# Kernel tuning notes

Measured on AMD Instinct MI355X. Metric: run time of the kernel, lower is better.

The kernel has to match this reference:

```python
import jax, jax.numpy as jnp
import numpy as np

B, L, C, H, W = 2, 4, 128, 48, 176
RATIO, DS = 0.4, 4.0   # voxel_size[0], downsample_rate
NUM_ITER = 2


def _make_pairwise_t(key):
    k1, k2 = jax.random.split(key)
    theta = jax.random.uniform(k1, (B, L, L), minval=-0.2, maxval=0.2)
    t = jax.random.uniform(k2, (B, L, L, 2), minval=-8.0, maxval=8.0)  # meters
    c, s = jnp.cos(theta), jnp.sin(theta)
    T = jnp.zeros((B, L, L, 4, 4), dtype=jnp.float32)
    T = T.at[..., 0, 0].set(c).at[..., 0, 1].set(-s)
    T = T.at[..., 1, 0].set(s).at[..., 1, 1].set(c)
    T = T.at[..., 0, 3].set(t[..., 0]).at[..., 1, 3].set(t[..., 1])
    T = T.at[..., 2, 2].set(1.0).at[..., 3, 3].set(1.0)
    d = jnp.arange(L)
    T = T.at[:, d, d].set(jnp.eye(4, dtype=jnp.float32))  # self-transform = identity
    return T


def setup_inputs():
    key = jax.random.key(0)
    ks = jax.random.split(key, 8)
    x = jax.random.normal(ks[0], (B, L, C, H, W), dtype=jnp.float32)
    record_len = jnp.array([L, L - 1], dtype=jnp.int32)
    mask = (jnp.arange(L)[None, :] < record_len[:, None]).astype(jnp.float32)
    pairwise_t_matrix = _make_pairwise_t(ks[1])
    W_msg = jax.random.normal(ks[2], (C, 2 * C, 3, 3), dtype=jnp.float32) * 0.021
    b_msg = jnp.zeros((C,), dtype=jnp.float32)
    W_gates = jax.random.normal(ks[3], (2 * C, 3 * C, 3, 3), dtype=jnp.float32) * 0.017
    b_gates = jnp.zeros((2 * C,), dtype=jnp.float32)
    W_can = jax.random.normal(ks[4], (C, 3 * C, 3, 3), dtype=jnp.float32) * 0.017
    b_can = jnp.zeros((C,), dtype=jnp.float32)
    W_mlp = jax.random.normal(ks[5], (C, C), dtype=jnp.float32) * 0.088
    b_mlp = jnp.zeros((C,), dtype=jnp.float32)
    return {"x": x, "mask": mask, "pairwise_t_matrix": pairwise_t_matrix,
            "record_len": record_len, "W_msg": W_msg, "b_msg": b_msg,
            "W_gates": W_gates, "b_gates": b_gates, "W_can": W_can,
            "b_can": b_can, "W_mlp": W_mlp, "b_mlp": b_mlp}


def _conv2d(x, w, b):
    y = jax.lax.conv_general_dilated(x, w, (1, 1), 'SAME',
                                     dimension_numbers=('NCHW', 'OIHW', 'NCHW'))
    return y + b[None, :, None, None]


def _affine_inv(T):
    # T: (..., 4, 4) neighbor->ego transform. Returns (..., 2, 3) inverse pixel
    # affine (maps dst pixel -> src pixel), i.e. get_discretized_transformation_matrix
    # + rotation-about-center + translation, then inverted (kornia warp_affine semantics).
    R = T[..., :2, :2]
    t = T[..., :2, 3] / (RATIO * DS)             # translation in pixels
    c = jnp.array([W / 2.0, H / 2.0], dtype=T.dtype)
    full_t = c - jnp.einsum('...ij,j->...i', R, c) + t   # (..., 2)
    det = R[..., 0, 0] * R[..., 1, 1] - R[..., 0, 1] * R[..., 1, 0]
    Rinv = jnp.stack([jnp.stack([R[..., 1, 1], -R[..., 0, 1]], -1),
                      jnp.stack([-R[..., 1, 0], R[..., 0, 0]], -1)], -2) / det[..., None, None]
    tinv = -jnp.einsum('...ij,...j->...i', Rinv, full_t)
    return jnp.concatenate([Rinv, tinv[..., None]], axis=-1)


def _warp_one(img, A):
    # img: (C, H, W); A: (2, 3) dst->src pixel map. Bilinear, zeros padding.
    ys, xs = jnp.meshgrid(jnp.arange(H, dtype=img.dtype),
                          jnp.arange(W, dtype=img.dtype), indexing='ij')
    sx = A[0, 0] * xs + A[0, 1] * ys + A[0, 2]
    sy = A[1, 0] * xs + A[1, 1] * ys + A[1, 2]
    x0 = jnp.floor(sx); y0 = jnp.floor(sy)
    wx1 = sx - x0; wy1 = sy - y0
    def gather(xi, yi):
        valid = ((xi >= 0) & (xi <= W - 1) & (yi >= 0) & (yi <= H - 1)).astype(img.dtype)
        xc = jnp.clip(xi, 0, W - 1).astype(jnp.int32)
        yc = jnp.clip(yi, 0, H - 1).astype(jnp.int32)
        return img[:, yc, xc] * valid
    return (gather(x0, y0) * (1 - wx1) * (1 - wy1)
            + gather(x0 + 1, y0) * wx1 * (1 - wy1)
            + gather(x0, y0 + 1) * (1 - wx1) * wy1
            + gather(x0 + 1, y0 + 1) * wx1 * wy1)


def _forward(x, mask, pairwise_t_matrix, record_len,
             W_msg, b_msg, W_gates, b_gates, W_can, b_can, W_mlp, b_mlp):
    # Ainv[b, j, i] warps neighbor j into ego i's frame; reorder to (b, i, j).
    Ainv = _affine_inv(pairwise_t_matrix)                      # (B, L, L, 2, 3)
    Ainv_bij = jnp.transpose(Ainv, (0, 2, 1, 3, 4)).reshape(-1, 2, 3)
    warp_v = jax.vmap(_warp_one)
    ones_img = jnp.ones((1, H, W), dtype=x.dtype)
    roi = jax.vmap(lambda A: _warp_one(ones_img, A))(Ainv_bij)  # (B*L*L, 1, H, W)
    com_mask = roi.reshape(B, L, L, 1, H, W) * mask[:, None, :, None, None, None]
    rec = record_len.astype(x.dtype)[:, None, None, None, None]
    feat = x
    for _ in range(NUM_ITER):
        nb = jnp.broadcast_to(feat[:, None], (B, L, L, C, H, W)).reshape(-1, C, H, W)
        warped = warp_v(nb, Ainv_bij).reshape(B, L, L, C, H, W)
        ego = jnp.broadcast_to(feat[:, :, None], (B, L, L, C, H, W))
        msg_in = jnp.concatenate([warped, ego], axis=3).reshape(-1, 2 * C, H, W)
        msg = _conv2d(msg_in, W_msg, b_msg).reshape(B, L, L, C, H, W) * com_mask
        agg = jnp.sum(msg, axis=2) / rec                        # mean over N valid cavs
        # ConvGRU, single layer / single step, zero-initialized hidden state
        gru_in = jnp.concatenate([feat, agg], axis=2).reshape(-1, 2 * C, H, W)
        h = jnp.zeros((B * L, C, H, W), dtype=x.dtype)
        gates = jax.nn.sigmoid(_conv2d(jnp.concatenate([gru_in, h], 1), W_gates, b_gates))
        r, u = jnp.split(gates, 2, axis=1)
        cand = jnp.tanh(_conv2d(jnp.concatenate([gru_in, r * h], 1), W_can, b_can))
        h = (1 - u) * h + u * cand
        feat = h.reshape(B, L, C, H, W)
    out = feat[:, 0]                                            # ego agent of each sample
    return jnp.einsum('bchw,oc->bohw', out, W_mlp) + b_mlp[None, :, None, None]


def reference(x, mask, pairwise_t_matrix, record_len,
              W_msg, b_msg, W_gates, b_gates, W_can, b_can, W_mlp, b_mlp):
    return _forward(x, mask, pairwise_t_matrix, record_len,
                    W_msg, b_msg, W_gates, b_gates, W_can, b_can, W_mlp, b_mlp)
```

## Files before the change

### kernel.cpp

```cpp
#include <hip/hip_runtime.h>
#include <math.h>

#define BB 2
#define LL 4
#define CC 128
#define HH 48
#define WWID 176
#define HW 8448

typedef _Float16 f16;
typedef __attribute__((ext_vector_type(8))) _Float16 f16x8;
typedef __attribute__((ext_vector_type(4))) _Float16 f16x4;
typedef __attribute__((ext_vector_type(2))) _Float16 f16x2;
typedef __attribute__((ext_vector_type(4))) float f32x4;
typedef __attribute__((ext_vector_type(4))) unsigned int u32x4;

__device__ __forceinline__ void ainv_from(const float* __restrict__ t, float* a)
{
    float R00=t[0], R01=t[1], t0=t[3];
    float R10=t[4], R11=t[5], t1=t[7];
    float tx = t0 * 0.625f;
    float ty = t1 * 0.625f;
    const float cx = WWID/2.0f, cy = HH/2.0f;
    float ftx = cx - (R00*cx + R01*cy) + tx;
    float fty = cy - (R10*cx + R11*cy) + ty;
    float det = R00*R11 - R01*R10;
    float inv = 1.0f/det;
    float i00 =  R11*inv, i01 = -R01*inv, i10 = -R10*inv, i11 = R00*inv;
    a[0]=i00; a[1]=i01; a[2]=-(i00*ftx + i01*fty);
    a[3]=i10; a[4]=i11; a[5]=-(i10*ftx + i11*fty);
}

__global__ __launch_bounds__(256)
void prep_kernel(const float* __restrict__ Wm, const float* __restrict__ Wg,
                 const float* __restrict__ Wc, const float* __restrict__ x,
                 const float* __restrict__ T, const float* __restrict__ mask,
                 f16* __restrict__ WmF, f16* __restrict__ WuF, f16* __restrict__ WcF,
                 f16* __restrict__ xT, float* __restrict__ fac)
{
    int bid = blockIdx.x;
    int tid = threadIdx.x;
    if (bid < 3456) {
        int which = bid / 1152;
        const float* src = (which==0) ? Wm : (which==1) ? Wg : Wc;
        f16* dst         = (which==0) ? WmF : (which==1) ? WuF : WcF;
        int oc_off = (which==1) ? 128 : 0;
        int stride = (which==0) ? 256 : 384;
        int idx = (bid % 1152)*256 + tid;
        int j     = idx & 7;
        int hi    = (idx >> 3) & 3;
        int l15   = (idx >> 5) & 15;
        int ocblk = (idx >> 9) & 7;
        int kq    = (idx >> 12) & 7;
        int tap   = idx >> 15;
        int oc  = ocblk*16 + l15;
        int cin = kq*32 + hi*8 + j;
        dst[idx] = (f16)src[((size_t)(oc_off+oc)*stride + cin)*9 + tap];
    } else if (bid < 3720) {
        int g = bid - 3456;
        int bl = g / 33;
        int pix = (g % 33)*256 + tid;
        const float* src = x + (size_t)bl*CC*HW + pix;
        f16* dst = xT + (size_t)bl*HW*CC + (size_t)pix*CC;
        for (int gg = 0; gg < 8; ++gg) {
            f16x8 v0, v1;
            #pragma unroll
            for (int c2 = 0; c2 < 8; ++c2) {
                v0[c2] = (f16)src[(size_t)(gg*16 + c2    )*HW];
                v1[c2] = (f16)src[(size_t)(gg*16 + 8 + c2)*HW];
            }
            *(f16x8*)(dst + gg*16    ) = v0;
            *(f16x8*)(dst + gg*16 + 8) = v1;
        }
    } else {
        int g = bid - 3720;
        int slot = g / 33;
        int pix = (g % 33)*256 + tid;
        int b = slot >> 4, l2 = (slot >> 2) & 3;
        float mk = mask[b*LL + l2];
        float a[6];
        ainv_from(T + slot*16, a);
        float gx = (float)(pix % WWID), gy = (float)(pix / WWID);
        float sx = a[0]*gx + a[1]*gy + a[2];
        float sy = a[3]*gx + a[4]*gy + a[5];
        float x0 = floorf(sx), y0 = floorf(sy);
        float wx = sx-x0, wy = sy-y0;
        int xi=(int)x0, yi=(int)y0;
        bool vx0 = xi>=0 && xi<WWID, vx1 = xi+1>=0 && xi+1<WWID;
        bool vy0 = yi>=0 && yi<HH,   vy1 = yi+1>=0 && yi+1<HH;
        float r = (vx0&&vy0?(1.f-wx)*(1.f-wy):0.f) + (vx1&&vy0?wx*(1.f-wy):0.f)
                + (vx0&&vy1?(1.f-wx)*wy:0.f)       + (vx1&&vy1?wx*wy:0.f);
        fac[(size_t)slot*HW + pix] = r*mk;
    }
}

template<int NM>
__global__ __launch_bounds__(256,3)
void msg_conv_kernel(const f16* __restrict__ featT, const float* __restrict__ T,
                     const float* __restrict__ fac, const float* __restrict__ mask,
                     const int* __restrict__ reclen,
                     const f16* __restrict__ WmF, const float* __restrict__ bm,
                     f16* __restrict__ Pm, int n_l1)
{
    int z = blockIdx.z;
    int b = z / (n_l1*5);
    int rem = z - b*(n_l1*5);
    int l1 = rem / 5, src = rem % 5;
    if (l1 != 0 && mask[b*LL + l1] == 0.f) return;
    bool ego = (src == 4);
    int l2 = ego ? l1 : src;
    if (!ego && mask[b*LL + l2] == 0.f) return;
    bool gather = (!ego) && (l2 != l1);
    int och = blockIdx.y;

    int ty = blockIdx.x / 11, tx = blockIdx.x % 11;
    int y0 = ty*8, x0 = tx*16;
    int tid = threadIdx.x;
    int wid = tid >> 6, lane = tid & 63;
    int wr = wid >> 1, wc = wid & 1;
    int l15 = lane & 15, hi = lane >> 4;

    __shared__ short lt[180*128];
    __shared__ float tw[4][192];
    __shared__ int   tof[4][192];

    const f16* in = featT + (size_t)(b*LL + l2)*HW*CC;

    if (gather) {
        float a6[6];
        ainv_from(T + ((b*LL + l2)*LL + l1)*16, a6);
        float a0=a6[0],a1=a6[1],a2=a6[2],a3=a6[3],a4=a6[4],a5=a6[5];
        for (int r = tid; r < 180; r += 256) {
            int yy = r / 18, xx = r - yy*18;
            int gy = y0 - 1 + yy, gx = x0 - 1 + xx;
            float w00=0.f,w10=0.f,w01=0.f,w11=0.f;
            int o00=0,o10=0,o01=0,o11=0;
            if (gy>=0 && gy<HH && gx>=0 && gx<WWID) {
                float sx = a0*(float)gx + a1*(float)gy + a2;
                float sy = a3*(float)gx + a4*(float)gy + a5;
                float xf = floorf(sx), yf = floorf(sy);
                float wx = sx-xf, wyv = sy-yf;
                int xi=(int)xf, yi=(int)yf;
                bool vx0=xi>=0&&xi<WWID, vx1=xi+1>=0&&xi+1<WWID;
                bool vy0=yi>=0&&yi<HH,   vy1=yi+1>=0&&yi+1<HH;
                int xc0=min(max(xi,0),WWID-1), xc1=min(max(xi+1,0),WWID-1);
                int yc0=min(max(yi,0),HH-1),   yc1=min(max(yi+1,0),HH-1);
                o00=(yc0*WWID+xc0)*CC; o10=(yc0*WWID+xc1)*CC;
                o01=(yc1*WWID+xc0)*CC; o11=(yc1*WWID+xc1)*CC;
                w00=(vx0&&vy0)?(1.f-wx)*(1.f-wyv):0.f;
                w10=(vx1&&vy0)?wx*(1.f-wyv):0.f;
                w01=(vx0&&vy1)?(1.f-wx)*wyv:0.f;
                w11=(vx1&&vy1)?wx*wyv:0.f;
            }
            tw[0][r]=w00; tw[1][r]=w10; tw[2][r]=w01; tw[3][r]=w11;
            tof[0][r]=o00; tof[1][r]=o10; tof[2][r]=o01; tof[3][r]=o11;
        }
        __syncthreads();
        for (int i = tid; i < 180*16; i += 256) {
            int row = i >> 4, cg = i & 15;
            f16 h00=(f16)tw[0][row], h10=(f16)tw[1][row];
            f16 h01=(f16)tw[2][row], h11=(f16)tw[3][row];
            f16x2 W00={h00,h00}, W10={h10,h10}, W01={h01,h01}, W11={h11,h11};
            int o00=tof[0][row], o10=tof[1][row], o01=tof[2][row], o11=tof[3][row];
            f16x8 t00 = *(const f16x8*)(in + o00 + cg*8);
            f16x8 t10 = *(const f16x8*)(in + o10 + cg*8);
            f16x8 t01 = *(const f16x8*)(in + o01 + cg*8);
            f16x8 t11 = *(const f16x8*)(in + o11 + cg*8);
            const f16x2* p00 = (const f16x2*)&t00;
            const f16x2* p10 = (const f16x2*)&t10;
            const f16x2* p01 = (const f16x2*)&t01;
            const f16x2* p11 = (const f16x2*)&t11;
            f16x8 outv;
            f16x2* po = (f16x2*)&outv;
            #pragma unroll
            for (int q=0;q<4;++q)
                po[q] = p00[q]*W00 + p10[q]*W10 + p01[q]*W01 + p11[q]*W11;
            int byte = row*256 + ((cg*16) ^ ((row&7)<<4));
            *(f16x8*)((char*)lt + byte) = outv;
        }
    } else {
        for (int i = tid; i < 180*16; i += 256) {
            int row = i >> 4, cg = i & 15;
            int yy = row / 18, xx = row - yy*18;
            int gy = y0 - 1 + yy, gx = x0 - 1 + xx;
            u32x4 val = {0,0,0,0};
            if (gy>=0 && gy<HH && gx>=0 && gx<WWID)
                val = *(const u32x4*)(in + (size_t)(gy*WWID+gx)*CC + cg*8);
            int byte = row*256 + ((cg*16) ^ ((row&7)<<4));
            *(u32x4*)((char*)lt + byte) = val;
        }
    }
    __syncthreads();

    f32x4 acc[NM][4];
    #pragma unroll
    for (int m=0;m<NM;++m)
        #pragma unroll
        for (int n=0;n<4;++n) acc[m][n] = (f32x4){0.f,0.f,0.f,0.f};

    const int kqbase = ego ? 4 : 0;
    const f16* wlane = WmF + l15*32 + hi*8;
    __builtin_amdgcn_s_setprio(1);
    for (int tap=0; tap<9; ++tap) {
        int dy = tap/3, dx = tap - dy*3;
        #pragma unroll
        for (int kk=0; kk<4; ++kk) {
            const f16* wt = wlane + (size_t)(((tap*8 + kqbase + kk)*8 + och*4 + wr*NM))*512;
            f16x8 av[NM];
            #pragma unroll
            for (int m=0;m<NM;++m)
                av[m] = *(const f16x8*)(wt + m*512);
            f16x8 bv[4];
            #pragma unroll
            for (int n=0;n<4;++n) {
                int pos = (wc*4 + n + dy)*18 + dx + l15;
                int byte = pos*256 + ((kk*64 + hi*16) ^ ((pos&7)<<4));
                bv[n] = *(const f16x8*)((const char*)lt + byte);
            }
            #pragma unroll
            for (int m=0;m<NM;++m)
                #pragma unroll
                for (int n=0;n<4;++n)
                    acc[m][n] = __builtin_amdgcn_mfma_f32_16x16x32_f16(
                        av[m], bv[n], acc[m][n], 0, 0, 0);
        }
    }
    __builtin_amdgcn_s_setprio(0);

    float invrec = 1.0f / (float)reclen[b];
    float fsc[4];
    if (ego) {
        #pragma unroll
        for (int n=0;n<4;++n) fsc[n] = 0.f;
        for (int j=0;j<LL;++j) {
            if (mask[b*LL + j] == 0.f) continue;
            const float* fp = fac + (size_t)(b*16 + j*4 + l1)*HW;
            #pragma unroll
            for (int n=0;n<4;++n)
                fsc[n] += fp[(y0 + wc*4 + n)*WWID + x0 + l15];
        }
    } else {
        const float* fp = fac + (size_t)(b*16 + l2*4 + l1)*HW;
        #pragma unroll
        for (int n=0;n<4;++n)
            fsc[n] = fp[(y0 + wc*4 + n)*WWID + x0 + l15];
    }
    #pragma unroll
    for (int n=0;n<4;++n) fsc[n] *= invrec;

    f16* outp = Pm + (size_t)z*HW*CC;
    #pragma unroll
    for (int m=0;m<NM;++m) {
        int oc = (och*4 + wr*NM + m)*16 + hi*4;
        f32x4 b4 = {0.f,0.f,0.f,0.f};
        if (ego) b4 = *(const f32x4*)(bm + oc);
        #pragma unroll
        for (int n=0;n<4;++n) {
            int pix = (y0 + wc*4 + n)*WWID + x0 + l15;
            f32x4 v = (acc[m][n] + b4) * fsc[n];
            f16x4 h = {(f16)v[0], (f16)v[1], (f16)v[2], (f16)v[3]};
            *(f16x4*)(outp + (size_t)pix*CC + oc) = h;
        }
    }
}

__global__ __launch_bounds__(256)
void reduce_agg_kernel(const f16* __restrict__ Pm, const float* __restrict__ mask,
                       f16* __restrict__ aggT, int n_l1)
{
    int zi = blockIdx.y;
    int b = zi / n_l1, l1 = zi % n_l1;
    if (l1 != 0 && mask[b*LL + l1] == 0.f) return;
    int idx = blockIdx.x*256 + threadIdx.x;
    int pix = idx >> 2, cgq = idx & 3;
    bool act[4];
    #pragma unroll
    for (int j=0;j<LL;++j) act[j] = (mask[b*LL + j] != 0.f);
    size_t off = (size_t)pix*CC + cgq*32;
    const f16* base = Pm + (size_t)(zi*5)*HW*CC + off;
    f16* dst = aggT + (size_t)zi*HW*CC + off;
    for (int cg=0; cg<4; ++cg) {
        float s[8];
        f16x8 e = *(const f16x8*)(base + (size_t)4*HW*CC + cg*8);
        #pragma unroll
        for (int j8=0;j8<8;++j8) s[j8] = (float)e[j8];
        #pragma unroll
        for (int j=0;j<4;++j) {
            if (!act[j]) continue;
            f16x8 p = *(const f16x8*)(base + (size_t)j*HW*CC + cg*8);
            #pragma unroll
            for (int j8=0;j8<8;++j8) s[j8] += (float)p[j8];
        }
        f16x8 o;
        #pragma unroll
        for (int j8=0;j8<8;++j8) o[j8] = (f16)s[j8];
        *(f16x8*)(dst + cg*8) = o;
    }
}

template<int NM>
__global__ __launch_bounds__(256,3)
void gru_conv_kernel(const f16* __restrict__ featT, const f16* __restrict__ aggT,
                     const float* __restrict__ mask,
                     const f16* __restrict__ WuF, const f16* __restrict__ WcF,
                     f16* __restrict__ Pg, int n_l1, int noc)
{
    int z = blockIdx.z;
    int b = z / n_l1, l1 = z % n_l1;
    if (l1 != 0 && mask[b*LL + l1] == 0.f) return;
    int gate = blockIdx.y / noc;
    int och  = blockIdx.y % noc;

    int ty = blockIdx.x / 11, tx = blockIdx.x % 11;
    int y0 = ty*8, x0 = tx*16;
    int tid = threadIdx.x;
    int wid = tid >> 6, lane = tid & 63;
    int wr = wid >> 1, wc = wid & 1;
    int l15 = lane & 15, hi = lane >> 4;

    __shared__ short lt[180*128];

    f32x4 acc[NM][4];
    #pragma unroll
    for (int m=0;m<NM;++m)
        #pragma unroll
        for (int n=0;n<4;++n) acc[m][n] = (f32x4){0.f,0.f,0.f,0.f};

    const f16* WF = (gate==0) ? WuF : WcF;
    const f16* wlane = WF + l15*32 + hi*8;

    for (int s = 0; s < 2; ++s) {
        const f16* in = (s==0) ? featT + (size_t)(b*LL + l1)*HW*CC
                               : aggT  + (size_t)(b*n_l1 + l1)*HW*CC;
        if (s) __syncthreads();
        for (int i = tid; i < 180*16; i += 256) {
            int row = i >> 4, cg = i & 15;
            int yy = row / 18, xx = row - yy*18;
            int gy = y0 - 1 + yy, gx = x0 - 1 + xx;
            u32x4 val = {0,0,0,0};
            if (gy>=0 && gy<HH && gx>=0 && gx<WWID)
                val = *(const u32x4*)(in + (size_t)(gy*WWID+gx)*CC + cg*8);
            int byte = row*256 + ((cg*16) ^ ((row&7)<<4));
            *(u32x4*)((char*)lt + byte) = val;
        }
        __syncthreads();

        int kqbase = s*4;
        __builtin_amdgcn_s_setprio(1);
        for (int tap=0; tap<9; ++tap) {
            int dy = tap/3, dx = tap - dy*3;
            #pragma unroll
            for (int kk=0; kk<4; ++kk) {
                const f16* wt = wlane + (size_t)(((tap*8 + kqbase + kk)*8 + och*4 + wr*NM))*512;
                f16x8 av[NM];
                #pragma unroll
                for (int m=0;m<NM;++m)
                    av[m] = *(const f16x8*)(wt + m*512);
                f16x8 bv[4];
                #pragma unroll
                for (int n=0;n<4;++n) {
                    int pos = (wc*4 + n + dy)*18 + dx + l15;
                    int byte = pos*256 + ((kk*64 + hi*16) ^ ((pos&7)<<4));
                    bv[n] = *(const f16x8*)((const char*)lt + byte);
                }
                #pragma unroll
                for (int m=0;m<NM;++m)
                    #pragma unroll
                    for (int n=0;n<4;++n)
                        acc[m][n] = __builtin_amdgcn_mfma_f32_16x16x32_f16(
                            av[m], bv[n], acc[m][n], 0, 0, 0);
            }
        }
        __builtin_amdgcn_s_setprio(0);
    }

    f16* outp = Pg + ((size_t)(gate*(BB*LL) + z))*HW*CC;
    #pragma unroll
    for (int m=0;m<NM;++m) {
        int oc = (och*4 + wr*NM + m)*16 + hi*4;
        #pragma unroll
        for (int n=0;n<4;++n) {
            int pix = (y0 + wc*4 + n)*WWID + x0 + l15;
            f32x4 v = acc[m][n];
            f16x4 h = {(f16)v[0], (f16)v[1], (f16)v[2], (f16)v[3]};
            *(f16x4*)(outp + (size_t)pix*CC + oc) = h;
        }
    }
}

__global__ __launch_bounds__(256)
void combine_kernel(const f16* __restrict__ Pg, const float* __restrict__ mask,
                    const float* __restrict__ bgU, const float* __restrict__ bc,
                    f16* __restrict__ outT, int n_l1)
{
    int z = blockIdx.y;
    int b = z / n_l1, l1 = z % n_l1;
    if (l1 != 0 && mask[b*LL + l1] == 0.f) return;
    int idx = blockIdx.x*256 + threadIdx.x;
    int pix = idx >> 2, cgq = idx & 3;
    size_t poff = (size_t)pix*CC + cgq*32;
    const f16* U = Pg + ((size_t)(0*(BB*LL) + z))*HW*CC + poff;
    const f16* C = Pg + ((size_t)(1*(BB*LL) + z))*HW*CC + poff;
    f16* dst = outT + (size_t)z*HW*CC + poff;
    for (int cg=0; cg<4; ++cg) {
        f16x8 u8 = *(const f16x8*)(U + cg*8);
        f16x8 c8 = *(const f16x8*)(C + cg*8);
        f16x8 o;
        #pragma unroll
        for (int j=0; j<8; ++j) {
            float uu = (float)u8[j] + bgU[cgq*32 + cg*8 + j];
            float cc = (float)c8[j] + bc[cgq*32 + cg*8 + j];
            float sig = 1.f/(1.f + expf(-uu));
            o[j] = (f16)(sig * tanhf(cc));
        }
        *(f16x8*)(dst + cg*8) = o;
    }
}

__global__ __launch_bounds__(256)
void mlp_kernel(const f16* __restrict__ Pg, const float* __restrict__ bgU,
                const float* __restrict__ bc, const float* __restrict__ Wm,
                const float* __restrict__ bmlp, float* __restrict__ out)
{
    int b = blockIdx.z, oc0 = blockIdx.y*32;
    int pix = blockIdx.x*256 + threadIdx.x;
    size_t poff = (size_t)pix*CC;
    const f16* U = Pg + ((size_t)(0*(BB*LL) + b))*HW*CC + poff;
    const f16* C = Pg + ((size_t)(1*(BB*LL) + b))*HW*CC + poff;
    float acc[32];
    #pragma unroll
    for (int oc=0;oc<32;++oc) acc[oc]=0.f;
    for (int c8 = 0; c8 < 16; ++c8) {
        f16x8 u8 = *(const f16x8*)(U + c8*8);
        f16x8 g8 = *(const f16x8*)(C + c8*8);
        float f[8];
        #pragma unroll
        for (int j=0;j<8;++j) {
            float uu = (float)u8[j] + bgU[c8*8 + j];
            float cc = (float)g8[j] + bc[c8*8 + j];
            float sig = 1.f/(1.f + expf(-uu));
            f[j] = sig * tanhf(cc);
        }
        #pragma unroll
        for (int oc=0; oc<32; ++oc) {
            const float* w = Wm + (size_t)(oc0+oc)*CC + c8*8;
            #pragma unroll
            for (int j=0;j<8;++j) acc[oc] = fmaf(f[j], w[j], acc[oc]);
        }
    }
    #pragma unroll
    for (int oc=0;oc<32;++oc)
        out[((size_t)b*CC + oc0+oc)*HW + pix] = acc[oc] + bmlp[oc0+oc];
}

extern "C" void kernel_launch(void* const* d_in, const int* in_sizes, int n_in,
                              void* d_out, int out_size, void* d_ws, size_t ws_size,
                              hipStream_t stream)
{
    const float* x     = (const float*)d_in[0];
    const float* mask  = (const float*)d_in[1];
    const float* T     = (const float*)d_in[2];
    const int*   recl  = (const int*)  d_in[3];
    const float* Wmsg  = (const float*)d_in[4];
    const float* bmsg  = (const float*)d_in[5];
    const float* Wg    = (const float*)d_in[6];
    const float* bg    = (const float*)d_in[7];
    const float* Wc    = (const float*)d_in[8];
    const float* bc    = (const float*)d_in[9];
    const float* Wmlp  = (const float*)d_in[10];
    const float* bmlp  = (const float*)d_in[11];
    float* out = (float*)d_out;

    char* w = (char*)d_ws;
    f16*   xT   = (f16*)w;            w += (size_t)BB*LL*HW*CC*2;
    float* fac  = (float*)w;          w += (size_t)32*HW*4;
    f16*   WmF  = (f16*)w;            w += (size_t)9*128*256*2;
    f16*   WuF  = (f16*)w;            w += (size_t)9*128*256*2;
    f16*   WcF  = (f16*)w;            w += (size_t)9*128*256*2;
    f16*   Pm   = (f16*)w;            w += (size_t)40*HW*CC*2;
    f16*   Pg   = (f16*)w;            w += (size_t)2*BB*LL*HW*CC*2;
    f16*   aggT = (f16*)w;            w += (size_t)BB*LL*HW*CC*2;
    f16*   f1T  = (f16*)w;            w += (size_t)BB*LL*HW*CC*2;

    prep_kernel<<<4776, 256, 0, stream>>>(Wmsg, Wg, Wc, x, T, mask,
                                          WmF, WuF, WcF, xT, fac);

    msg_conv_kernel<4><<<dim3(66, 1, BB*LL*5), 256, 0, stream>>>(
        xT, T, fac, mask, recl, WmF, bmsg, Pm, LL);
    reduce_agg_kernel<<<dim3(132, BB*LL), 256, 0, stream>>>(Pm, mask, aggT, LL);
    gru_conv_kernel<4><<<dim3(66, 2, BB*LL), 256, 0, stream>>>(
        xT, aggT, mask, WuF, WcF, Pg, LL, 1);
    combine_kernel<<<dim3(132, BB*LL), 256, 0, stream>>>(
        Pg, mask, bg + CC, bc, f1T, LL);

    msg_conv_kernel<2><<<dim3(66, 2, BB*5), 256, 0, stream>>>(
        f1T, T, fac, mask, recl, WmF, bmsg, Pm, 1);
    reduce_agg_kernel<<<dim3(132, BB), 256, 0, stream>>>(Pm, mask, aggT, 1);
    gru_conv_kernel<2><<<dim3(66, 4, BB), 256, 0, stream>>>(
        f1T, aggT, mask, WuF, WcF, Pg, 1, 2);

    mlp_kernel<<<dim3(33, 4, BB), 256, 0, stream>>>(
        Pg, bg + CC, bc, Wmlp, bmlp, out);
}
```

Before: 461.0 us.

## Fuse GRU update and candidate convs with the gate epilogue in one kernel

The GRU conv kernel now computes the update-gate and candidate convolutions together for the same output channels, sharing one LDS input tile. It then applies sigmoid·tanh in the epilogue and writes the new hidden state directly. This removes the separate combine kernel and the round trip of the two pre-activation tensors through global memory, and the final MLP now reads the finished feature map. The NM tiling is halved to keep two accumulator sets within register limits, which changes per-block work and may raise register pressure or lower occupancy.

```diff
diff --git a/kernel.cpp b/kernel.cpp
--- a/kernel.cpp
+++ b/kernel.cpp
@@ -205,7 +205,7 @@
         int dy = tap/3, dx = tap - dy*3;
         #pragma unroll
         for (int kk=0; kk<4; ++kk) {
-            const f16* wt = wlane + (size_t)(((tap*8 + kqbase + kk)*8 + och*4 + wr*NM))*512;
+            const f16* wt = wlane + (size_t)(((tap*8 + kqbase + kk)*8 + och*(2*NM) + wr*NM))*512;
             f16x8 av[NM];
             #pragma unroll
             for (int m=0;m<NM;++m)
@@ -251,7 +251,7 @@
     f16* outp = Pm + (size_t)z*HW*CC;
     #pragma unroll
     for (int m=0;m<NM;++m) {
-        int oc = (och*4 + wr*NM + m)*16 + hi*4;
+        int oc = (och*(2*NM) + wr*NM + m)*16 + hi*4;
         f32x4 b4 = {0.f,0.f,0.f,0.f};
         if (ego) b4 = *(const f32x4*)(bm + oc);
         #pragma unroll
@@ -303,13 +303,13 @@
 void gru_conv_kernel(const f16* __restrict__ featT, const f16* __restrict__ aggT,
                      const float* __restrict__ mask,
                      const f16* __restrict__ WuF, const f16* __restrict__ WcF,
-                     f16* __restrict__ Pg, int n_l1, int noc)
+                     const float* __restrict__ bgU, const float* __restrict__ bc,
+                     f16* __restrict__ outT, int n_l1)
 {
     int z = blockIdx.z;
     int b = z / n_l1, l1 = z % n_l1;
     if (l1 != 0 && mask[b*LL + l1] == 0.f) return;
-    int gate = blockIdx.y / noc;
-    int och  = blockIdx.y % noc;
+    int och = blockIdx.y;
 
     int ty = blockIdx.x / 11, tx = blockIdx.x % 11;
     int y0 = ty*8, x0 = tx*16;
@@ -320,14 +320,17 @@
 
     __shared__ short lt[180*128];
 
-    f32x4 acc[NM][4];
+    f32x4 aU[NM][4], aC[NM][4];
     #pragma unroll
     for (int m=0;m<NM;++m)
         #pragma unroll
-        for (int n=0;n<4;++n) acc[m][n] = (f32x4){0.f,0.f,0.f,0.f};
-
-    const f16* WF = (gate==0) ? WuF : WcF;
-    const f16* wlane = WF + l15*32 + hi*8;
+        for (int n=0;n<4;++n) {
+            aU[m][n] = (f32x4){0.f,0.f,0.f,0.f};
+            aC[m][n] = (f32x4){0.f,0.f,0.f,0.f};
+        }
+
+    const f16* wlaneU = WuF + l15*32 + hi*8;
+    const f16* wlaneC = WcF + l15*32 + hi*8;
 
     for (int s = 0; s < 2; ++s) {
         const f16* in = (s==0) ? featT + (size_t)(b*LL + l1)*HW*CC
@@ -351,11 +354,13 @@
             int dy = tap/3, dx = tap - dy*3;
             #pragma unroll
             for (int kk=0; kk<4; ++kk) {
-                const f16* wt = wlane + (size_t)(((tap*8 + kqbase + kk)*8 + och*4 + wr*NM))*512;
-                f16x8 av[NM];
+                size_t blkoff = (size_t)(((tap*8 + kqbase + kk)*8 + och*(2*NM) + wr*NM))*512;
+                f16x8 avU[NM], avC[NM];
                 #pragma unroll
-                for (int m=0;m<NM;++m)
-                    av[m] = *(const f16x8*)(wt + m*512);
+                for (int m=0;m<NM;++m) {
+                    avU[m] = *(const f16x8*)(wlaneU + blkoff + m*512);
+                    avC[m] = *(const f16x8*)(wlaneC + blkoff + m*512);
+                }
                 f16x8 bv[4];
                 #pragma unroll
                 for (int n=0;n<4;++n) {
@@ -366,81 +371,54 @@
                 #pragma unroll
                 for (int m=0;m<NM;++m)
                     #pragma unroll
-                    for (int n=0;n<4;++n)
-                        acc[m][n] = __builtin_amdgcn_mfma_f32_16x16x32_f16(
-                            av[m], bv[n], acc[m][n], 0, 0, 0);
+                    for (int n=0;n<4;++n) {
+                        aU[m][n] = __builtin_amdgcn_mfma_f32_16x16x32_f16(
+                            avU[m], bv[n], aU[m][n], 0, 0, 0);
+                        aC[m][n] = __builtin_amdgcn_mfma_f32_16x16x32_f16(
+                            avC[m], bv[n], aC[m][n], 0, 0, 0);
+                    }
             }
         }
         __builtin_amdgcn_s_setprio(0);
     }
 
-    f16* outp = Pg + ((size_t)(gate*(BB*LL) + z))*HW*CC;
+    f16* outp = outT + (size_t)z*HW*CC;
     #pragma unroll
     for (int m=0;m<NM;++m) {
-        int oc = (och*4 + wr*NM + m)*16 + hi*4;
+        int oc = (och*(2*NM) + wr*NM + m)*16 + hi*4;
+        f32x4 bu4 = *(const f32x4*)(bgU + oc);
+        f32x4 bc4 = *(const f32x4*)(bc  + oc);
         #pragma unroll
         for (int n=0;n<4;++n) {
             int pix = (y0 + wc*4 + n)*WWID + x0 + l15;
-            f32x4 v = acc[m][n];
-            f16x4 h = {(f16)v[0], (f16)v[1], (f16)v[2], (f16)v[3]};
+            f32x4 u4 = aU[m][n] + bu4;
+            f32x4 c4 = aC[m][n] + bc4;
+            f16x4 h;
+            #pragma unroll
+            for (int j=0;j<4;++j) {
+                float sig = 1.f/(1.f + expf(-u4[j]));
+                h[j] = (f16)(sig * tanhf(c4[j]));
+            }
             *(f16x4*)(outp + (size_t)pix*CC + oc) = h;
         }
     }
 }
 
 __global__ __launch_bounds__(256)
-void combine_kernel(const f16* __restrict__ Pg, const float* __restrict__ mask,
-                    const float* __restrict__ bgU, const float* __restrict__ bc,
-                    f16* __restrict__ outT, int n_l1)
-{
-    int z = blockIdx.y;
-    int b = z / n_l1, l1 = z % n_l1;
-    if (l1 != 0 && mask[b*LL + l1] == 0.f) return;
-    int idx = blockIdx.x*256 + threadIdx.x;
-    int pix = idx >> 2, cgq = idx & 3;
-    size_t poff = (size_t)pix*CC + cgq*32;
-    const f16* U = Pg + ((size_t)(0*(BB*LL) + z))*HW*CC + poff;
-    const f16* C = Pg + ((size_t)(1*(BB*LL) + z))*HW*CC + poff;
-    f16* dst = outT + (size_t)z*HW*CC + poff;
-    for (int cg=0; cg<4; ++cg) {
-        f16x8 u8 = *(const f16x8*)(U + cg*8);
-        f16x8 c8 = *(const f16x8*)(C + cg*8);
-        f16x8 o;
-        #pragma unroll
-        for (int j=0; j<8; ++j) {
-            float uu = (float)u8[j] + bgU[cgq*32 + cg*8 + j];
-            float cc = (float)c8[j] + bc[cgq*32 + cg*8 + j];
-            float sig = 1.f/(1.f + expf(-uu));
-            o[j] = (f16)(sig * tanhf(cc));
-        }
-        *(f16x8*)(dst + cg*8) = o;
-    }
-}
-
-__global__ __launch_bounds__(256)
-void mlp_kernel(const f16* __restrict__ Pg, const float* __restrict__ bgU,
-                const float* __restrict__ bc, const float* __restrict__ Wm,
+void mlp_kernel(const f16* __restrict__ feat2T, const float* __restrict__ Wm,
                 const float* __restrict__ bmlp, float* __restrict__ out)
 {
     int b = blockIdx.z, oc0 = blockIdx.y*32;
     int pix = blockIdx.x*256 + threadIdx.x;
-    size_t poff = (size_t)pix*CC;
-    const f16* U = Pg + ((size_t)(0*(BB*LL) + b))*HW*CC + poff;
-    const f16* C = Pg + ((size_t)(1*(BB*LL) + b))*HW*CC + poff;
+    const f16* src = feat2T + (size_t)b*HW*CC + (size_t)pix*CC;
     float acc[32];
     #pragma unroll
     for (int oc=0;oc<32;++oc) acc[oc]=0.f;
     for (int c8 = 0; c8 < 16; ++c8) {
-        f16x8 u8 = *(const f16x8*)(U + c8*8);
-        f16x8 g8 = *(const f16x8*)(C + c8*8);
+        f16x8 v = *(const f16x8*)(src + c8*8);
         float f[8];
         #pragma unroll
-        for (int j=0;j<8;++j) {
-            float uu = (float)u8[j] + bgU[c8*8 + j];
-            float cc = (float)g8[j] + bc[c8*8 + j];
-            float sig = 1.f/(1.f + expf(-uu));
-            f[j] = sig * tanhf(cc);
-        }
+        for (int j=0;j<8;++j) f[j] = (float)v[j];
         #pragma unroll
         for (int oc=0; oc<32; ++oc) {
             const float* w = Wm + (size_t)(oc0+oc)*CC + c8*8;
@@ -478,9 +456,9 @@
     f16*   WuF  = (f16*)w;            w += (size_t)9*128*256*2;
     f16*   WcF  = (f16*)w;            w += (size_t)9*128*256*2;
     f16*   Pm   = (f16*)w;            w += (size_t)40*HW*CC*2;
-    f16*   Pg   = (f16*)w;            w += (size_t)2*BB*LL*HW*CC*2;
     f16*   aggT = (f16*)w;            w += (size_t)BB*LL*HW*CC*2;
     f16*   f1T  = (f16*)w;            w += (size_t)BB*LL*HW*CC*2;
+    f16*   f2T  = (f16*)w;            w += (size_t)BB*HW*CC*2;
 
     prep_kernel<<<4776, 256, 0, stream>>>(Wmsg, Wg, Wc, x, T, mask,
                                           WmF, WuF, WcF, xT, fac);
@@ -488,17 +466,14 @@
     msg_conv_kernel<4><<<dim3(66, 1, BB*LL*5), 256, 0, stream>>>(
         xT, T, fac, mask, recl, WmF, bmsg, Pm, LL);
     reduce_agg_kernel<<<dim3(132, BB*LL), 256, 0, stream>>>(Pm, mask, aggT, LL);
-    gru_conv_kernel<4><<<dim3(66, 2, BB*LL), 256, 0, stream>>>(
-        xT, aggT, mask, WuF, WcF, Pg, LL, 1);
-    combine_kernel<<<dim3(132, BB*LL), 256, 0, stream>>>(
-        Pg, mask, bg + CC, bc, f1T, LL);
+    gru_conv_kernel<2><<<dim3(66, 2, BB*LL), 256, 0, stream>>>(
+        xT, aggT, mask, WuF, WcF, bg + CC, bc, f1T, LL);
 
     msg_conv_kernel<2><<<dim3(66, 2, BB*5), 256, 0, stream>>>(
         f1T, T, fac, mask, recl, WmF, bmsg, Pm, 1);
     reduce_agg_kernel<<<dim3(132, BB), 256, 0, stream>>>(Pm, mask, aggT, 1);
-    gru_conv_kernel<2><<<dim3(66, 4, BB), 256, 0, stream>>>(
-        f1T, aggT, mask, WuF, WcF, Pg, 1, 2);
-
-    mlp_kernel<<<dim3(33, 4, BB), 256, 0, stream>>>(
-        Pg, bg + CC, bc, Wmlp, bmlp, out);
-}
+    gru_conv_kernel<1><<<dim3(66, 4, BB), 256, 0, stream>>>(
+        f1T, aggT, mask, WuF, WcF, bg + CC, bc, f2T, 1);
+
+    mlp_kernel<<<dim3(33, 4, BB), 256, 0, stream>>>(f2T, Wmlp, bmlp, out);
+}
```

After: 424.3 us (median of 2 runs). 8.0% less time.
